# Kernel tuning notes

Hardware: AMD Instinct MI355X
Metric: run time of the kernel (lower is better)

Reference implementation:

```python
import jax, jax.numpy as jnp
import numpy as np
from jax import lax

B, S, CIN, COUT = 32, 1024, 256, 256
EPS = 1e-5
LA = 0.1  # ResidualAttention la


def _cnorm(x, w, b):
    # ChannelNorm: mean/var over channel dim (axis=1); torch.var is unbiased (ddof=1)
    m = jnp.mean(x, axis=1, keepdims=True)
    v = jnp.var(x, axis=1, keepdims=True, ddof=1)
    return (x - m) * lax.rsqrt(v + EPS) * w[None, :, None] + b[None, :, None]


def _conv1d(x, w, pad):
    # x: [B, C_in, L], w: [C_out, C_in, K]
    return lax.conv_general_dilated(x, w, (1,), [(pad, pad)],
                                    dimension_numbers=('NCH', 'OIH', 'NCH'))


def _gate(x, fc_w):
    # ResidualAttention: 1x1 conv to 2 classes, mean + la*max over class dim, sigmoid
    y = _conv1d(x, fc_w, 0)                                   # [B, 2, L]
    score = jax.nn.sigmoid(jnp.mean(y, axis=1) + LA * jnp.max(y, axis=1))  # [B, L]
    return x * (1.0 + score[:, None, :])


def _pad_to(x, s):
    # pad_after_conv: zero-pad time dim back to s
    return jnp.pad(x, ((0, 0), (0, 0), (0, s - x.shape[-1])))


def _block(x, cn_w, cn_b, W, pad, fc_w, s):
    h = _conv1d(jax.nn.relu(_cnorm(x, cn_w, cn_b)), W, pad)
    return _pad_to(_gate(h, fc_w), s)


def setup_inputs() -> dict:
    key = jax.random.key(0)
    ks = jax.random.split(key, 8)
    d = {"inputs": jax.random.normal(ks[0], (B, S, CIN), jnp.float32)}
    cins = {4: CIN, 5: COUT, 6: COUT, 7: COUT, 8: COUT}
    for i, k in enumerate(range(4, 9)):
        cin = cins[k]
        d[f"cn{k}_w"] = jnp.ones((cin,), jnp.float32)
        d[f"cn{k}_b"] = jnp.zeros((cin,), jnp.float32)
        d[f"W{k}"] = jax.random.normal(ks[i + 1], (COUT, cin, k), jnp.float32) * (1.0 / np.sqrt(cin * k))
    d["fc_w"] = jax.random.normal(ks[6], (2, COUT, 1), jnp.float32) * (1.0 / np.sqrt(COUT))
    return d


def reference(inputs, cn4_w, cn4_b, W4, cn5_w, cn5_b, W5, cn6_w, cn6_b, W6,
              cn7_w, cn7_b, W7, cn8_w, cn8_b, W8, fc_w):
    x = jnp.transpose(inputs, (0, 2, 1))  # [B, C, S]
    s = x.shape[-1]
    # torch padding: int((k-1)/2) -> k=4:1, k=5:2, k=6:2, k=7:3, k=8:3
    x = _block(x, cn4_w, cn4_b, W4, 1, fc_w, s)
    x = _block(x, cn5_w, cn5_b, W5, 2, fc_w, s)
    x = _block(x, cn6_w, cn6_b, W6, 2, fc_w, s)
    x = _block(x, cn7_w, cn7_b, W7, 3, fc_w, s)
    x = _block(x, cn8_w, cn8_b, W8, 3, fc_w, s)
    return jnp.transpose(x, (0, 2, 1))  # [B, S, C_out]
```

## Files before the change

kernel.cpp:

```cpp
#include <hip/hip_runtime.h>
#include <hip/hip_bf16.h>

#define B_ 32
#define S_ 1024
#define C_ 256
#define SP 1040

typedef float f32x4  __attribute__((ext_vector_type(4)));
typedef float f32x16 __attribute__((ext_vector_type(16)));
typedef __bf16 bf16x8 __attribute__((ext_vector_type(8)));
typedef __bf16 bf16x4 __attribute__((ext_vector_type(4)));

__global__ __launch_bounds__(256) void wcvt_kernel(const float* __restrict__ w,
                                                   __hip_bfloat16* __restrict__ wb,
                                                   int k, int n) {
    int i = blockIdx.x * 256 + threadIdx.x;
    if (i >= n) return;
    int e   = i & 7;
    int co  = (i >> 3) & 255;
    int hh  = (i >> 11) & 1;
    int ks  = (i >> 12) & 1;
    int c32 = (i >> 13) & 7;
    int j   = i >> 16;
    int ci  = c32 * 32 + ks * 16 + hh * 8 + e;
    wb[i] = __float2bfloat16(w[(co * 256 + ci) * k + j]);
}

template<bool GATE, bool NORM, bool BF16IN>
__global__ __launch_bounds__(256) void prep_kernel(const void* __restrict__ in_,
                                                   const float* __restrict__ fc,
                                                   const float* __restrict__ cw,
                                                   const float* __restrict__ cb,
                                                   __hip_bfloat16* __restrict__ yout,
                                                   float* __restrict__ fout) {
    const int lane = threadIdx.x & 63;
    const int rid  = blockIdx.x * 4 + (threadIdx.x >> 6);

    int b, t;
    __hip_bfloat16* drow = nullptr;
    if constexpr (NORM) {
        b = rid / SP;
        const int r = rid - b * SP;
        t = r - 8;
        drow = yout + ((size_t)(b * SP + r)) * C_ + lane * 4;
        if (t < 0 || t >= S_) {
            *(ushort4*)drow = make_ushort4(0, 0, 0, 0);
            return;
        }
    } else {
        b = rid >> 10;
        t = rid & 1023;
    }

    f32x4 xv;
    if constexpr (BF16IN) {
        const __hip_bfloat16* row = (const __hip_bfloat16*)in_ + ((size_t)(b * S_ + t)) * C_;
        bf16x4 hv = *(const bf16x4*)(row + lane * 4);
        xv.x = (float)hv[0]; xv.y = (float)hv[1]; xv.z = (float)hv[2]; xv.w = (float)hv[3];
    } else {
        const float* row = (const float*)in_ + ((size_t)(b * S_ + t)) * C_;
        xv = *(const f32x4*)(row + lane * 4);
    }

    if constexpr (GATE) {
        f32x4 f0 = *(const f32x4*)(fc + lane * 4);
        f32x4 f1 = *(const f32x4*)(fc + C_ + lane * 4);
        float p = xv.x * f0.x + xv.y * f0.y + xv.z * f0.z + xv.w * f0.w;
        float q = xv.x * f1.x + xv.y * f1.y + xv.z * f1.z + xv.w * f1.w;
#pragma unroll
        for (int m = 32; m >= 1; m >>= 1) {
            p += __shfl_xor(p, m, 64);
            q += __shfl_xor(q, m, 64);
        }
        float s = 0.5f * (p + q) + 0.1f * fmaxf(p, q);
        float score = 1.0f / (1.0f + expf(-s));
        float gmul = 1.0f + score;
        xv.x *= gmul; xv.y *= gmul; xv.z *= gmul; xv.w *= gmul;
    }

    if constexpr (NORM) {
        float s1 = xv.x + xv.y + xv.z + xv.w;
        float s2 = xv.x * xv.x + xv.y * xv.y + xv.z * xv.z + xv.w * xv.w;
#pragma unroll
        for (int m = 32; m >= 1; m >>= 1) {
            s1 += __shfl_xor(s1, m, 64);
            s2 += __shfl_xor(s2, m, 64);
        }
        float mean = s1 * (1.0f / 256.0f);
        float var  = fmaxf((s2 - 256.0f * mean * mean) * (1.0f / 255.0f), 0.0f);
        float inv  = rsqrtf(var + 1e-5f);
        f32x4 w4 = *(const f32x4*)(cw + lane * 4);
        f32x4 b4 = *(const f32x4*)(cb + lane * 4);
        float v0 = fmaxf(0.0f, (xv.x - mean) * inv * w4.x + b4.x);
        float v1 = fmaxf(0.0f, (xv.y - mean) * inv * w4.y + b4.y);
        float v2 = fmaxf(0.0f, (xv.z - mean) * inv * w4.z + b4.z);
        float v3 = fmaxf(0.0f, (xv.w - mean) * inv * w4.w + b4.w);
        union { ushort4 u; __hip_bfloat16 e[4]; } o;
        o.e[0] = __float2bfloat16(v0);
        o.e[1] = __float2bfloat16(v1);
        o.e[2] = __float2bfloat16(v2);
        o.e[3] = __float2bfloat16(v3);
        *(ushort4*)drow = o.u;
    } else {
        *(f32x4*)(fout + ((size_t)(b * S_ + t)) * C_ + lane * 4) = xv;
    }
}

template<int KS, int PAD, int LVALID>
__global__ __launch_bounds__(512) void conv_kernel(const __hip_bfloat16* __restrict__ y,
                                                   const __hip_bfloat16* __restrict__ wb,
                                                   __hip_bfloat16* __restrict__ hout) {
    __shared__ alignas(16) __hip_bfloat16 ly[72 * 2 * 256];
    const int tid  = threadIdx.x;
    const int lane = tid & 63;
    const int wv   = tid >> 6;
    const int tt   = blockIdx.x & 15;
    const int bp   = blockIdx.x >> 4;
    const int t0   = tt << 6;
    const int b2   = bp * 2;

#pragma unroll
    for (int c = 0; c < 9; ++c) {
        int u = c * 512 + tid;
        int r = u >> 6, q = u & 63;
        int bbs = q >> 5, s = q & 31;
        const __hip_bfloat16* src = y + ((size_t)((b2 + bbs) * SP + 8 + t0 - PAD + r)) * C_
                                      + ((s ^ (r & 7)) << 3);
        *(bf16x8*)(ly + (size_t)u * 8) = *(const bf16x8*)src;
    }
    __syncthreads();

    const int bb      = wv & 1;
    const int co_base = (wv >> 1) * 64;
    const int l31     = lane & 31;
    const int hh      = lane >> 5;

    f32x16 acc[2][2];
#pragma unroll
    for (int mf = 0; mf < 2; ++mf)
#pragma unroll
        for (int nf = 0; nf < 2; ++nf)
#pragma unroll
            for (int e = 0; e < 16; ++e)
                acc[mf][nf][e] = 0.0f;

    const __hip_bfloat16* abase = wb + (size_t)hh * 2048 + (size_t)(co_base + l31) * 8;
    const __hip_bfloat16* lbb   = ly + bb * 256;

#pragma unroll 4
    for (int s = 0; s < KS * 8; ++s) {
        const int j   = s >> 3;
        const int c32 = s & 7;
        bf16x8 a[2][2], bf[2][2];
#pragma unroll
        for (int ks = 0; ks < 2; ++ks)
#pragma unroll
            for (int mf = 0; mf < 2; ++mf)
                a[ks][mf] = *(const bf16x8*)(abase + (size_t)(s * 4 + ks * 2) * 2048 + mf * 256);
#pragma unroll
        for (int ks = 0; ks < 2; ++ks)
#pragma unroll
            for (int nf = 0; nf < 2; ++nf) {
                int r   = nf * 32 + l31 + j;
                int ci8 = c32 * 4 + ks * 2 + hh;
                bf[ks][nf] = *(const bf16x8*)(lbb + (size_t)r * 512 + ((ci8 ^ (r & 7)) << 3));
            }
#pragma unroll
        for (int ks = 0; ks < 2; ++ks)
#pragma unroll
            for (int mf = 0; mf < 2; ++mf)
#pragma unroll
                for (int nf = 0; nf < 2; ++nf)
                    acc[mf][nf] = __builtin_amdgcn_mfma_f32_32x32x16_bf16(
                        a[ks][mf], bf[ks][nf], acc[mf][nf], 0, 0, 0);
    }

    __hip_bfloat16* hb = hout + ((size_t)((b2 + bb) * S_ + t0)) * C_ + co_base;
#pragma unroll
    for (int nf = 0; nf < 2; ++nf) {
        int tl = nf * 32 + l31;
        bool zout = (LVALID < S_) && (t0 + tl >= LVALID);
#pragma unroll
        for (int mf = 0; mf < 2; ++mf) {
#pragma unroll
            for (int r4 = 0; r4 < 4; ++r4) {
                int co = mf * 32 + r4 * 8 + hh * 4;
                union { ushort4 u; __hip_bfloat16 e[4]; } o;
#pragma unroll
                for (int q = 0; q < 4; ++q) {
                    float v = zout ? 0.0f : acc[mf][nf][r4 * 4 + q];
                    o.e[q] = __float2bfloat16(v);
                }
                *(ushort4*)(hb + (size_t)tl * C_ + co) = o.u;
            }
        }
    }
}

extern "C" void kernel_launch(void* const* d_in, const int* in_sizes, int n_in,
                              void* d_out, int out_size, void* d_ws, size_t ws_size,
                              hipStream_t stream) {
    const float* inputs = (const float*)d_in[0];
    const float* cw[5] = { (const float*)d_in[1],  (const float*)d_in[4],
                           (const float*)d_in[7],  (const float*)d_in[10],
                           (const float*)d_in[13] };
    const float* cb[5] = { (const float*)d_in[2],  (const float*)d_in[5],
                           (const float*)d_in[8],  (const float*)d_in[11],
                           (const float*)d_in[14] };
    const float* Wf[5] = { (const float*)d_in[3],  (const float*)d_in[6],
                           (const float*)d_in[9],  (const float*)d_in[12],
                           (const float*)d_in[15] };
    const float* fc = (const float*)d_in[16];

    char* ws = (char*)d_ws;
    __hip_bfloat16* y = (__hip_bfloat16*)ws;
    __hip_bfloat16* h = (__hip_bfloat16*)(ws + 17039360);
    __hip_bfloat16* wb[5];
    size_t off = 17039360 + 16777216;
    for (int l = 0; l < 5; ++l) {
        wb[l] = (__hip_bfloat16*)(ws + off);
        off += (size_t)(l + 4) * 65536 * 2;
    }
    float* out = (float*)d_out;

    for (int l = 0; l < 5; ++l) {
        int k = l + 4, n = k * 65536;
        wcvt_kernel<<<(n + 255) / 256, 256, 0, stream>>>(Wf[l], wb[l], k, n);
    }

    const int GN = (B_ * SP) / 4;
    prep_kernel<false, true, false><<<GN, 256, 0, stream>>>(inputs, fc, cw[0], cb[0], y, nullptr);
    conv_kernel<4, 1, 1023><<<256, 512, 0, stream>>>(y, wb[0], h);
    prep_kernel<true, true, true><<<GN, 256, 0, stream>>>(h, fc, cw[1], cb[1], y, nullptr);
    conv_kernel<5, 2, 1024><<<256, 512, 0, stream>>>(y, wb[1], h);
    prep_kernel<true, true, true><<<GN, 256, 0, stream>>>(h, fc, cw[2], cb[2], y, nullptr);
    conv_kernel<6, 2, 1023><<<256, 512, 0, stream>>>(y, wb[2], h);
    prep_kernel<true, true, true><<<GN, 256, 0, stream>>>(h, fc, cw[3], cb[3], y, nullptr);
    conv_kernel<7, 3, 1024><<<256, 512, 0, stream>>>(y, wb[3], h);
    prep_kernel<true, true, true><<<GN, 256, 0, stream>>>(h, fc, cw[4], cb[4], y, nullptr);
    conv_kernel<8, 3, 1023><<<256, 512, 0, stream>>>(y, wb[4], h);
    prep_kernel<true, false, true><<<(B_ * S_) / 4, 256, 0, stream>>>(h, fc, nullptr, nullptr, nullptr, out);
}
```

Before: 374.7 us.

## Retile conv to 256-step x 128-channel blocks and batch four rows per prep wave

The conv kernel now tiles one batch, 256 time steps and 128 output channels per block instead of two batches, 64 time steps and all channels. The halo overhead in the shared input tile shrinks, but each input tile is loaded twice, once per channel half. It adds launch_bounds occupancy 2 and per-tap __syncthreads, which look unnecessary because shared memory is read-only after the load. The prep kernel processes four rows per wave to batch its shuffle reductions and loads, with a quarter as many blocks.

```diff
diff --git a/kernel.cpp b/kernel.cpp
--- a/kernel.cpp
+++ b/kernel.cpp
@@ -34,106 +34,140 @@
                                                    __hip_bfloat16* __restrict__ yout,
                                                    float* __restrict__ fout) {
     const int lane = threadIdx.x & 63;
-    const int rid  = blockIdx.x * 4 + (threadIdx.x >> 6);
-
-    int b, t;
-    __hip_bfloat16* drow = nullptr;
-    if constexpr (NORM) {
-        b = rid / SP;
-        const int r = rid - b * SP;
-        t = r - 8;
-        drow = yout + ((size_t)(b * SP + r)) * C_ + lane * 4;
-        if (t < 0 || t >= S_) {
-            *(ushort4*)drow = make_ushort4(0, 0, 0, 0);
-            return;
-        }
-    } else {
-        b = rid >> 10;
-        t = rid & 1023;
-    }
-
-    f32x4 xv;
-    if constexpr (BF16IN) {
-        const __hip_bfloat16* row = (const __hip_bfloat16*)in_ + ((size_t)(b * S_ + t)) * C_;
-        bf16x4 hv = *(const bf16x4*)(row + lane * 4);
-        xv.x = (float)hv[0]; xv.y = (float)hv[1]; xv.z = (float)hv[2]; xv.w = (float)hv[3];
-    } else {
-        const float* row = (const float*)in_ + ((size_t)(b * S_ + t)) * C_;
-        xv = *(const f32x4*)(row + lane * 4);
+    const int rid0 = (blockIdx.x * 4 + (threadIdx.x >> 6)) * 4;
+
+    f32x4 xv[4];
+    int bi[4], ti[4];
+    bool live[4];
+
+#pragma unroll
+    for (int rr = 0; rr < 4; ++rr) {
+        int rid = rid0 + rr;
+        if constexpr (NORM) {
+            int b = rid / SP;
+            int r = rid - b * SP;
+            int t = r - 8;
+            bi[rr] = b; ti[rr] = t;
+            live[rr] = (t >= 0) && (t < S_);
+            if (!live[rr])
+                *(ushort4*)(yout + (size_t)rid * C_ + lane * 4) = make_ushort4(0, 0, 0, 0);
+        } else {
+            bi[rr] = rid >> 10; ti[rr] = rid & 1023; live[rr] = true;
+        }
+    }
+
+#pragma unroll
+    for (int rr = 0; rr < 4; ++rr) {
+        if (live[rr]) {
+            size_t idx = ((size_t)(bi[rr] * S_ + ti[rr])) * C_ + lane * 4;
+            if constexpr (BF16IN) {
+                bf16x4 hv = *(const bf16x4*)((const __hip_bfloat16*)in_ + idx);
+                xv[rr].x = (float)hv[0]; xv[rr].y = (float)hv[1];
+                xv[rr].z = (float)hv[2]; xv[rr].w = (float)hv[3];
+            } else {
+                xv[rr] = *(const f32x4*)((const float*)in_ + idx);
+            }
+        } else {
+            xv[rr] = f32x4{0.f, 0.f, 0.f, 0.f};
+        }
     }
 
     if constexpr (GATE) {
         f32x4 f0 = *(const f32x4*)(fc + lane * 4);
         f32x4 f1 = *(const f32x4*)(fc + C_ + lane * 4);
-        float p = xv.x * f0.x + xv.y * f0.y + xv.z * f0.z + xv.w * f0.w;
-        float q = xv.x * f1.x + xv.y * f1.y + xv.z * f1.z + xv.w * f1.w;
+        float p[4], q[4];
+#pragma unroll
+        for (int rr = 0; rr < 4; ++rr) {
+            p[rr] = xv[rr].x * f0.x + xv[rr].y * f0.y + xv[rr].z * f0.z + xv[rr].w * f0.w;
+            q[rr] = xv[rr].x * f1.x + xv[rr].y * f1.y + xv[rr].z * f1.z + xv[rr].w * f1.w;
+        }
 #pragma unroll
         for (int m = 32; m >= 1; m >>= 1) {
-            p += __shfl_xor(p, m, 64);
-            q += __shfl_xor(q, m, 64);
-        }
-        float s = 0.5f * (p + q) + 0.1f * fmaxf(p, q);
-        float score = 1.0f / (1.0f + expf(-s));
-        float gmul = 1.0f + score;
-        xv.x *= gmul; xv.y *= gmul; xv.z *= gmul; xv.w *= gmul;
+#pragma unroll
+            for (int rr = 0; rr < 4; ++rr) {
+                p[rr] += __shfl_xor(p[rr], m, 64);
+                q[rr] += __shfl_xor(q[rr], m, 64);
+            }
+        }
+#pragma unroll
+        for (int rr = 0; rr < 4; ++rr) {
+            float s = 0.5f * (p[rr] + q[rr]) + 0.1f * fmaxf(p[rr], q[rr]);
+            float g = 1.0f + 1.0f / (1.0f + expf(-s));
+            xv[rr].x *= g; xv[rr].y *= g; xv[rr].z *= g; xv[rr].w *= g;
+        }
     }
 
     if constexpr (NORM) {
-        float s1 = xv.x + xv.y + xv.z + xv.w;
-        float s2 = xv.x * xv.x + xv.y * xv.y + xv.z * xv.z + xv.w * xv.w;
+        float s1[4], s2[4];
+#pragma unroll
+        for (int rr = 0; rr < 4; ++rr) {
+            s1[rr] = xv[rr].x + xv[rr].y + xv[rr].z + xv[rr].w;
+            s2[rr] = xv[rr].x * xv[rr].x + xv[rr].y * xv[rr].y
+                   + xv[rr].z * xv[rr].z + xv[rr].w * xv[rr].w;
+        }
 #pragma unroll
         for (int m = 32; m >= 1; m >>= 1) {
-            s1 += __shfl_xor(s1, m, 64);
-            s2 += __shfl_xor(s2, m, 64);
-        }
-        float mean = s1 * (1.0f / 256.0f);
-        float var  = fmaxf((s2 - 256.0f * mean * mean) * (1.0f / 255.0f), 0.0f);
-        float inv  = rsqrtf(var + 1e-5f);
+#pragma unroll
+            for (int rr = 0; rr < 4; ++rr) {
+                s1[rr] += __shfl_xor(s1[rr], m, 64);
+                s2[rr] += __shfl_xor(s2[rr], m, 64);
+            }
+        }
         f32x4 w4 = *(const f32x4*)(cw + lane * 4);
         f32x4 b4 = *(const f32x4*)(cb + lane * 4);
-        float v0 = fmaxf(0.0f, (xv.x - mean) * inv * w4.x + b4.x);
-        float v1 = fmaxf(0.0f, (xv.y - mean) * inv * w4.y + b4.y);
-        float v2 = fmaxf(0.0f, (xv.z - mean) * inv * w4.z + b4.z);
-        float v3 = fmaxf(0.0f, (xv.w - mean) * inv * w4.w + b4.w);
-        union { ushort4 u; __hip_bfloat16 e[4]; } o;
-        o.e[0] = __float2bfloat16(v0);
-        o.e[1] = __float2bfloat16(v1);
-        o.e[2] = __float2bfloat16(v2);
-        o.e[3] = __float2bfloat16(v3);
-        *(ushort4*)drow = o.u;
+#pragma unroll
+        for (int rr = 0; rr < 4; ++rr) {
+            if (!live[rr]) continue;
+            float mean = s1[rr] * (1.0f / 256.0f);
+            float var  = fmaxf((s2[rr] - 256.0f * mean * mean) * (1.0f / 255.0f), 0.0f);
+            float inv  = rsqrtf(var + 1e-5f);
+            union { ushort4 u; __hip_bfloat16 e[4]; } o;
+            o.e[0] = __float2bfloat16(fmaxf(0.0f, (xv[rr].x - mean) * inv * w4.x + b4.x));
+            o.e[1] = __float2bfloat16(fmaxf(0.0f, (xv[rr].y - mean) * inv * w4.y + b4.y));
+            o.e[2] = __float2bfloat16(fmaxf(0.0f, (xv[rr].z - mean) * inv * w4.z + b4.z));
+            o.e[3] = __float2bfloat16(fmaxf(0.0f, (xv[rr].w - mean) * inv * w4.w + b4.w));
+            *(ushort4*)(yout + (size_t)(rid0 + rr) * C_ + lane * 4) = o.u;
+        }
     } else {
-        *(f32x4*)(fout + ((size_t)(b * S_ + t)) * C_ + lane * 4) = xv;
+#pragma unroll
+        for (int rr = 0; rr < 4; ++rr) {
+            *(f32x4*)(fout + ((size_t)(bi[rr] * S_ + ti[rr])) * C_ + lane * 4) = xv[rr];
+        }
     }
 }
 
 template<int KS, int PAD, int LVALID>
-__global__ __launch_bounds__(512) void conv_kernel(const __hip_bfloat16* __restrict__ y,
-                                                   const __hip_bfloat16* __restrict__ wb,
-                                                   __hip_bfloat16* __restrict__ hout) {
-    __shared__ alignas(16) __hip_bfloat16 ly[72 * 2 * 256];
+__global__ __launch_bounds__(512, 2) void conv_kernel(const __hip_bfloat16* __restrict__ y,
+                                                      const __hip_bfloat16* __restrict__ wb,
+                                                      __hip_bfloat16* __restrict__ hout) {
+    __shared__ alignas(16) __hip_bfloat16 ly[264 * 256];
     const int tid  = threadIdx.x;
     const int lane = tid & 63;
     const int wv   = tid >> 6;
-    const int tt   = blockIdx.x & 15;
-    const int bp   = blockIdx.x >> 4;
-    const int t0   = tt << 6;
-    const int b2   = bp * 2;
-
-#pragma unroll
-    for (int c = 0; c < 9; ++c) {
-        int u = c * 512 + tid;
-        int r = u >> 6, q = u & 63;
-        int bbs = q >> 5, s = q & 31;
-        const __hip_bfloat16* src = y + ((size_t)((b2 + bbs) * SP + 8 + t0 - PAD + r)) * C_
-                                      + ((s ^ (r & 7)) << 3);
-        *(bf16x8*)(ly + (size_t)u * 8) = *(const bf16x8*)src;
+    const int cg   = blockIdx.x & 1;
+    const int tt   = (blockIdx.x >> 1) & 3;
+    const int b    = blockIdx.x >> 3;
+    const int t0   = tt << 8;
+
+    {
+        const __hip_bfloat16* ybase = y + ((size_t)(b * SP + 8 + t0 - PAD)) * C_;
+#pragma unroll
+        for (int c = 0; c < 17; ++c) {
+            int u = c * 512 + tid;
+            if (u < 8448) {
+                int r = u >> 5, s = u & 31;
+                bf16x8 v = *(const bf16x8*)(ybase + (size_t)r * C_ + ((s ^ (r & 7)) << 3));
+                *(bf16x8*)(ly + (size_t)u * 8) = v;
+            }
+        }
     }
     __syncthreads();
 
-    const int bb      = wv & 1;
-    const int co_base = (wv >> 1) * 64;
-    const int l31     = lane & 31;
-    const int hh      = lane >> 5;
+    const int cog = wv & 1;
+    const int tq  = wv >> 1;
+    const int l31 = lane & 31;
+    const int hh  = lane >> 5;
+    const int co_base = cg * 128 + cog * 64;
 
     f32x16 acc[2][2];
 #pragma unroll
@@ -145,41 +179,42 @@
                 acc[mf][nf][e] = 0.0f;
 
     const __hip_bfloat16* abase = wb + (size_t)hh * 2048 + (size_t)(co_base + l31) * 8;
-    const __hip_bfloat16* lbb   = ly + bb * 256;
-
+
+    for (int j = 0; j < KS; ++j) {
+        if (j) __syncthreads();
 #pragma unroll 4
-    for (int s = 0; s < KS * 8; ++s) {
-        const int j   = s >> 3;
-        const int c32 = s & 7;
-        bf16x8 a[2][2], bf[2][2];
-#pragma unroll
-        for (int ks = 0; ks < 2; ++ks)
-#pragma unroll
-            for (int mf = 0; mf < 2; ++mf)
-                a[ks][mf] = *(const bf16x8*)(abase + (size_t)(s * 4 + ks * 2) * 2048 + mf * 256);
-#pragma unroll
-        for (int ks = 0; ks < 2; ++ks)
-#pragma unroll
-            for (int nf = 0; nf < 2; ++nf) {
-                int r   = nf * 32 + l31 + j;
-                int ci8 = c32 * 4 + ks * 2 + hh;
-                bf[ks][nf] = *(const bf16x8*)(lbb + (size_t)r * 512 + ((ci8 ^ (r & 7)) << 3));
-            }
-#pragma unroll
-        for (int ks = 0; ks < 2; ++ks)
-#pragma unroll
-            for (int mf = 0; mf < 2; ++mf)
-#pragma unroll
-                for (int nf = 0; nf < 2; ++nf)
-                    acc[mf][nf] = __builtin_amdgcn_mfma_f32_32x32x16_bf16(
-                        a[ks][mf], bf[ks][nf], acc[mf][nf], 0, 0, 0);
-    }
-
-    __hip_bfloat16* hb = hout + ((size_t)((b2 + bb) * S_ + t0)) * C_ + co_base;
+        for (int c32 = 0; c32 < 8; ++c32) {
+            const int s = j * 8 + c32;
+            bf16x8 a[2][2], bf[2][2];
+#pragma unroll
+            for (int ks = 0; ks < 2; ++ks)
+#pragma unroll
+                for (int mf = 0; mf < 2; ++mf)
+                    a[ks][mf] = *(const bf16x8*)(abase + (size_t)(s * 4 + ks * 2) * 2048 + mf * 256);
+#pragma unroll
+            for (int ks = 0; ks < 2; ++ks)
+#pragma unroll
+                for (int nf = 0; nf < 2; ++nf) {
+                    int r   = tq * 64 + nf * 32 + l31 + j;
+                    int ci8 = c32 * 4 + ks * 2 + hh;
+                    bf[ks][nf] = *(const bf16x8*)(ly + (size_t)r * 256 + ((ci8 ^ (r & 7)) << 3));
+                }
+#pragma unroll
+            for (int ks = 0; ks < 2; ++ks)
+#pragma unroll
+                for (int mf = 0; mf < 2; ++mf)
+#pragma unroll
+                    for (int nf = 0; nf < 2; ++nf)
+                        acc[mf][nf] = __builtin_amdgcn_mfma_f32_32x32x16_bf16(
+                            a[ks][mf], bf[ks][nf], acc[mf][nf], 0, 0, 0);
+        }
+    }
+
+    __hip_bfloat16* hb = hout + ((size_t)(b * S_ + t0 + tq * 64)) * C_ + co_base;
 #pragma unroll
     for (int nf = 0; nf < 2; ++nf) {
         int tl = nf * 32 + l31;
-        bool zout = (LVALID < S_) && (t0 + tl >= LVALID);
+        bool zout = (LVALID < S_) && (t0 + tq * 64 + tl >= LVALID);
 #pragma unroll
         for (int mf = 0; mf < 2; ++mf) {
 #pragma unroll
@@ -228,7 +263,8 @@
         wcvt_kernel<<<(n + 255) / 256, 256, 0, stream>>>(Wf[l], wb[l], k, n);
     }
 
-    const int GN = (B_ * SP) / 4;
+    const int GN = (B_ * SP) / 16;
+    const int GO = (B_ * S_) / 16;
     prep_kernel<false, true, false><<<GN, 256, 0, stream>>>(inputs, fc, cw[0], cb[0], y, nullptr);
     conv_kernel<4, 1, 1023><<<256, 512, 0, stream>>>(y, wb[0], h);
     prep_kernel<true, true, true><<<GN, 256, 0, stream>>>(h, fc, cw[1], cb[1], y, nullptr);
@@ -239,5 +275,5 @@
     conv_kernel<7, 3, 1024><<<256, 512, 0, stream>>>(y, wb[3], h);
     prep_kernel<true, true, true><<<GN, 256, 0, stream>>>(h, fc, cw[4], cb[4], y, nullptr);
     conv_kernel<8, 3, 1023><<<256, 512, 0, stream>>>(y, wb[4], h);
-    prep_kernel<true, false, true><<<(B_ * S_) / 4, 256, 0, stream>>>(h, fc, nullptr, nullptr, nullptr, out);
-}
+    prep_kernel<true, false, true><<<GO, 256, 0, stream>>>(h, fc, nullptr, nullptr, nullptr, out);
+}
```

New measurement: 406.8 us. 8.6% more time.
